# Kernel tuning notes

Hardware: AMD Instinct MI355X
Metric: run time of the kernel (lower is better)

Reference implementation:

```python
import jax, jax.numpy as jnp
import numpy as np

B, N, DIM = 64, 64, 256
HEADS, P = 4, 16
H, W, C = 56, 56, 256
CH = C // HEADS            # per-head channels = eff_in_dim = eff_out_dim = 64
IN_PTS = HEADS * P         # 64
OUT_PTS = IN_PTS           # 64
TOTAL = CH * CH + IN_PTS * OUT_PTS  # 8192
GRAD_NORM = 1.0 / H

# RestrictGradNorm: identity fwd, clamp grad in bwd
@jax.custom_vjp
def restrict_grad(x):
    return x

def _rg_fwd(x):
    return x, None

def _rg_bwd(_, g):
    return (jnp.clip(g, -GRAD_NORM, GRAD_NORM),)

restrict_grad.defvjp(_rg_fwd, _rg_bwd)


def grid_sample_bilinear(feat, grid):
    # feat [G,c,h,w], grid [G,Hg,Wg,2] in [-1,1]; align_corners=False, zeros padding
    G, c, h, w = feat.shape
    Hg, Wg = grid.shape[1], grid.shape[2]
    Q = Hg * Wg
    x = (grid[..., 0] + 1.0) * 0.5 * w - 0.5
    y = (grid[..., 1] + 1.0) * 0.5 * h - 0.5
    x0f = jnp.floor(x); y0f = jnp.floor(y)
    wx1 = x - x0f; wx0 = 1.0 - wx1
    wy1 = y - y0f; wy0 = 1.0 - wy1
    x0 = x0f.astype(jnp.int32); y0 = y0f.astype(jnp.int32)
    fflat = feat.reshape(G, c, h * w)

    def gather(xi, yi):
        valid = (xi >= 0) & (xi < w) & (yi >= 0) & (yi < h)
        idx = (jnp.clip(yi, 0, h - 1) * w + jnp.clip(xi, 0, w - 1)).reshape(G, Q)
        v = jnp.take_along_axis(fflat, jnp.broadcast_to(idx[:, None, :], (G, c, Q)), axis=2)
        return v * valid.reshape(G, 1, Q)

    out = (gather(x0, y0) * (wx0 * wy0).reshape(G, 1, Q)
           + gather(x0 + 1, y0) * (wx1 * wy0).reshape(G, 1, Q)
           + gather(x0, y0 + 1) * (wx0 * wy1).reshape(G, 1, Q)
           + gather(x0 + 1, y0 + 1) * (wx1 * wy1).reshape(G, 1, Q))
    return out.reshape(G, c, Hg, Wg)


def setup_inputs() -> dict:
    key = jax.random.key(0)
    ks = jax.random.split(key, 10)
    img_feat = jax.random.normal(ks[0], (B, C, H, W), jnp.float32)
    ctr = jax.random.uniform(ks[1], (B, N, 2), jnp.float32) * 0.8 + 0.1
    wh = jax.random.uniform(ks[2], (B, N, 2), jnp.float32) * 0.4 + 0.1
    token_roi = jnp.concatenate([ctr - wh / 2, ctr + wh / 2], axis=-1)
    query = jax.random.normal(ks[3], (B, N, DIM), jnp.float32)
    W_off = jax.random.normal(ks[4], (DIM, HEADS * P * 2), jnp.float32) * 0.02
    b_off = jnp.zeros((HEADS * P * 2,), jnp.float32)
    ln_w = jnp.ones((DIM,), jnp.float32)
    ln_b = jnp.zeros((DIM,), jnp.float32)
    W1 = jax.random.normal(ks[5], (DIM, DIM // 4), jnp.float32) * 0.02
    b1 = jnp.zeros((DIM // 4,), jnp.float32)
    W2 = jax.random.normal(ks[6], (DIM // 4, TOTAL), jnp.float32) * 0.02
    b2 = jax.random.normal(ks[7], (TOTAL,), jnp.float32) * 0.02
    m_beta = jnp.zeros((CH,), jnp.float32)
    s_beta = jnp.zeros((OUT_PTS,), jnp.float32)
    W_out = jax.random.normal(ks[8], (CH * OUT_PTS, DIM), jnp.float32) * 0.02
    b_out = jnp.zeros((DIM,), jnp.float32)
    return dict(img_feat=img_feat, token_roi=token_roi, query=query, W_off=W_off,
                b_off=b_off, ln_w=ln_w, ln_b=ln_b, W1=W1, b1=b1, W2=W2, b2=b2,
                m_beta=m_beta, s_beta=s_beta, W_out=W_out, b_out=b_out)


def _forward(img_feat, token_roi, query, W_off, b_off, ln_w, ln_b, W1, b1, W2, b2,
             m_beta, s_beta, W_out, b_out):
    # 1) sampling offsets from query
    off = (query @ W_off + b_off).reshape(B, N, 1, IN_PTS, 2)
    # 2) make_absolute_sampling_point: normalize over points (unbiased std, as torch)
    mean = off.mean(axis=-2, keepdims=True)
    std = jnp.std(off, axis=-2, ddof=1, keepdims=True) + 1e-7
    off = (off - mean) / (3.0 * std)
    roi_xy = (token_roi[:, :, 2:] + token_roi[:, :, :2]) * 0.5   # [B,N,2]
    roi_wh = token_roi[:, :, 2:] - token_roi[:, :, :2]
    pts = roi_xy[:, :, None, None, :] + off * roi_wh[:, :, None, None, :]  # [B,N,1,HP,2]
    # 3) sampling_from_img_feat: per-head bilinear grid sample
    sp = pts.reshape(B, N, 1, HEADS, P, 2).transpose(0, 3, 1, 2, 4, 5)
    sp = sp.reshape(B * HEADS, N, P, 2)
    sp = restrict_grad(sp)
    grid = sp * 2.0 - 1.0
    feat = img_feat.reshape(B * HEADS, CH, H, W)
    out = grid_sample_bilinear(feat, grid)                        # [B*HEADS, CH, N, P]
    out = out.reshape(B, HEADS, CH, N, 1, P).transpose(0, 3, 4, 1, 5, 2)
    sampled = out.reshape(B * N, IN_PTS, CH)                      # g==1 in AdaptiveMixing
    # 4) AdaptiveMixing: parameter generator (LN eps 1e-6 -> Linear -> Linear)
    mu = query.mean(-1, keepdims=True)
    var = query.var(-1, keepdims=True)
    qn = (query - mu) / jnp.sqrt(var + 1e-6) * ln_w + ln_b
    params = ((qn @ W1 + b1) @ W2 + b2).reshape(B * N, TOTAL)
    cm = params[:, :CH * CH].reshape(B * N, CH, CH)               # channel mixing
    sm = params[:, CH * CH:].reshape(B * N, OUT_PTS, IN_PTS)      # spatial mixing
    x = jax.nn.gelu(jnp.einsum('bpc,bcd->bpd', sampled, cm) + m_beta, approximate=False)
    x = jax.nn.gelu(jnp.einsum('bop,bpc->boc', sm, x) + s_beta[None, :, None], approximate=False)
    x = x.reshape(B, N, OUT_PTS * CH) @ W_out + b_out
    return x


def reference(img_feat, token_roi, query, W_off, b_off, ln_w, ln_b, W1, b1, W2, b2,
              m_beta, s_beta, W_out, b_out):
    return _forward(img_feat, token_roi, query, W_off, b_off, ln_w, ln_b, W1, b1,
                    W2, b2, m_beta, s_beta, W_out, b_out)
```

## Files before the change

### kernel.cpp

```cpp
#include <hip/hip_runtime.h>


typedef unsigned short u16;
typedef u16 u16x8 __attribute__((ext_vector_type(8)));
typedef u16 u16x4 __attribute__((ext_vector_type(4)));
typedef short bf16x8 __attribute__((ext_vector_type(8)));
typedef float f32x4 __attribute__((ext_vector_type(4)));
#define SA 72
#define MFMA(a, b, c) __builtin_amdgcn_mfma_f32_16x16x32_bf16(a, b, c, 0, 0, 0)

static __device__ __forceinline__ float bf2f(u16 s) {
    union { float f; unsigned u; } v; v.u = ((unsigned)s) << 16; return v.f;
}
static __device__ __forceinline__ u16 f2bf(float f) {
    union { float f; unsigned u; } v; v.f = f;
    unsigned r = v.u + 0x7fffu + ((v.u >> 16) & 1u);
    return (u16)(r >> 16);
}
static __device__ __forceinline__ float gelu(float x) {
    const float z  = x * 0.70710678118654752f;
    const float az = fabsf(z);
    const float t  = 1.0f / fmaf(0.3275911f, az, 1.0f);
    float p = fmaf(t, 1.061405429f, -1.453152027f);
    p = fmaf(t, p, 1.421413741f);
    p = fmaf(t, p, -0.284496736f);
    p = fmaf(t, p, 0.254829592f);
    p = p * t;
    const float e    = __expf(-z * z);
    const float erfa = fmaf(-p, e, 1.0f);
    const float erfz = copysignf(erfa, z);
    return 0.5f * x * (1.0f + erfz);
}
static __device__ __forceinline__ float loadf(const void* p, size_t i, int isbf) {
    return isbf ? bf2f(((const u16*)p)[i]) : ((const float*)p)[i];
}
static __device__ __forceinline__ int detect_bf(const void* ln_w) {
    return (*(const unsigned*)ln_w == 0x3F800000u) ? 0 : 1;
}


static __device__ void body_trans(const void* __restrict__ src, u16* __restrict__ dst,
                                  int R, int C, int c0, int r0, int isbf,
                                  float* __restrict__ tile) {
    const int tid = threadIdx.x;
#pragma unroll
    for (int i = 0; i < 16; i++) {
        int e = i * 256 + tid;
        int rr = e >> 6, cc = e & 63;
        tile[rr * 65 + cc] = loadf(src, (size_t)(r0 + rr) * C + c0 + cc, isbf);
    }
    __syncthreads();
#pragma unroll
    for (int i = 0; i < 16; i++) {
        int e = i * 256 + tid;
        int cc = e >> 6, rr = e & 63;
        dst[(size_t)(c0 + cc) * R + r0 + rr] = f2bf(tile[rr * 65 + cc]);
    }
}

static __device__ void body_k0(const void* __restrict__ img, u16* __restrict__ featT,
                               int pos0, int c0, int bz, int isbf,
                               u16* __restrict__ tile ) {
    const int tid = threadIdx.x;
    if (isbf) {
        const u16* ib = (const u16*)img;
#pragma unroll
        for (int i = 0; i < 2; i++) {
            const int e = i * 256 + tid;
            const int ch = e >> 3, g = e & 7;
            const int gs = g ^ (ch & 7) ^ ((ch >> 3) & 7);
            u16x8 v = *(const u16x8*)&ib[((size_t)bz * 256 + c0 + ch) * 3136 + pos0 + g * 8];
            *(u16x8*)&tile[ch * SA + gs * 8] = v;
        }
    } else {
        const float* ifp = (const float*)img;
#pragma unroll
        for (int i = 0; i < 4; i++) {
            const int e = i * 256 + tid;
            const int ch = e >> 4, pq = (e & 15) * 4;
            const int g = pq >> 3, gs = g ^ (ch & 7) ^ ((ch >> 3) & 7);
            f32x4 v = *(const f32x4*)&ifp[((size_t)bz * 256 + c0 + ch) * 3136 + pos0 + pq];
            u16x4 o;
#pragma unroll
            for (int j = 0; j < 4; j++) o[j] = f2bf(v[j]);
            *(u16x4*)&tile[ch * SA + gs * 8 + (pq & 7)] = o;
        }
    }
    __syncthreads();
#pragma unroll
    for (int i = 0; i < 2; i++) {
        const int e = i * 256 + tid;
        const int pos = e >> 3, cb = (e & 7) * 8;
        const int pg = pos >> 3, pe = pos & 7;
        u16x8 v;
#pragma unroll
        for (int j = 0; j < 8; j++) {
            const int row = cb + j;
            const int sw = pg ^ (row & 7) ^ ((row >> 3) & 7);
            v[j] = tile[row * SA + sw * 8 + pe];
        }
        *(u16x8*)&featT[((size_t)bz * 3136 + pos0 + pos) * 256 + c0 + cb] = v;
    }
}

static __device__ void body_k1(const void* __restrict__ query, const void* __restrict__ roi,
                               const void* __restrict__ W_off, const void* __restrict__ b_off,
                               const void* __restrict__ ln_w, const void* __restrict__ ln_b,
                               const void* __restrict__ W1, const void* __restrict__ b1,
                               int isbf, int t,
                               float* __restrict__ pts, u16* __restrict__ hbuf,
                               float* __restrict__ smem) {
    float* qf    = smem;
    float* qn    = smem + 256;
    float* offl  = smem + 512;
    float* red   = smem + 640;
    float* stats = smem + 648;
    const int tid = threadIdx.x;
    float q = loadf(query, (size_t)t * 256 + tid, isbf);
    qf[tid] = q;
    float v = q;
#pragma unroll
    for (int o = 32; o; o >>= 1) v += __shfl_down(v, o, 64);
    if ((tid & 63) == 0) red[tid >> 6] = v;
    __syncthreads();
    if (tid == 0) stats[0] = (red[0] + red[1] + red[2] + red[3]) * (1.f / 256.f);
    __syncthreads();
    float mu = stats[0];
    float dv = q - mu;
    v = dv * dv;
#pragma unroll
    for (int o = 32; o; o >>= 1) v += __shfl_down(v, o, 64);
    if ((tid & 63) == 0) red[tid >> 6] = v;
    __syncthreads();
    if (tid == 0) stats[1] = (red[0] + red[1] + red[2] + red[3]) * (1.f / 256.f);
    __syncthreads();
    float inv = rsqrtf(stats[1] + 1e-6f);
    qn[tid] = dv * inv * loadf(ln_w, tid, isbf) + loadf(ln_b, tid, isbf);
    __syncthreads();
    if (tid < 128) {
        float a0 = 0.f, a1 = 0.f, a2 = 0.f, a3 = 0.f;
        for (int d = 0; d < 256; d += 4) {
            a0 = fmaf(qf[d],     loadf(W_off, (size_t)d * 128 + tid, isbf),       a0);
            a1 = fmaf(qf[d + 1], loadf(W_off, (size_t)(d + 1) * 128 + tid, isbf), a1);
            a2 = fmaf(qf[d + 2], loadf(W_off, (size_t)(d + 2) * 128 + tid, isbf), a2);
            a3 = fmaf(qf[d + 3], loadf(W_off, (size_t)(d + 3) * 128 + tid, isbf), a3);
        }
        offl[tid] = ((a0 + a1) + (a2 + a3)) + loadf(b_off, tid, isbf);
    } else if (tid < 192) {
        int k = tid - 128;
        float a0 = 0.f, a1 = 0.f, a2 = 0.f, a3 = 0.f;
        for (int d = 0; d < 256; d += 4) {
            a0 = fmaf(qn[d],     loadf(W1, (size_t)d * 64 + k, isbf),       a0);
            a1 = fmaf(qn[d + 1], loadf(W1, (size_t)(d + 1) * 64 + k, isbf), a1);
            a2 = fmaf(qn[d + 2], loadf(W1, (size_t)(d + 2) * 64 + k, isbf), a2);
            a3 = fmaf(qn[d + 3], loadf(W1, (size_t)(d + 3) * 64 + k, isbf), a3);
        }
        hbuf[(size_t)t * 64 + k] = f2bf(((a0 + a1) + (a2 + a3)) + loadf(b1, k, isbf));
    }
    __syncthreads();
    const float ov = (tid < 128) ? offl[tid] : 0.f;
    {
        float s = ov;
#pragma unroll
        for (int o = 2; o < 64; o <<= 1) s += __shfl_xor(s, o, 64);
        if (tid < 128 && (tid & 63) < 2) red[(tid >> 6) * 2 + (tid & 1)] = s;
    }
    __syncthreads();
    const int xy = tid & 1;
    const float m = (red[xy] + red[2 + xy]) * (1.f / 64.f);
    {
        float d = (tid < 128) ? ov - m : 0.f;
        float sq = d * d;
#pragma unroll
        for (int o = 2; o < 64; o <<= 1) sq += __shfl_xor(sq, o, 64);
        if (tid < 128 && (tid & 63) < 2) red[4 + (tid >> 6) * 2 + (tid & 1)] = sq;
    }
    __syncthreads();
    if (tid < 128) {
        float s2 = red[4 + xy] + red[6 + xy];
        float sd = sqrtf(s2 * (1.f / 63.f));
        float inv3 = 1.f / (3.f * (sd + 1e-7f));
        float lo = loadf(roi, (size_t)t * 4 + xy, isbf);
        float hi = loadf(roi, (size_t)t * 4 + 2 + xy, isbf);
        pts[(size_t)t * 128 + tid] = 0.5f * (lo + hi) + (ov - m) * inv3 * (hi - lo);
    }
}

static __device__ void body_k2t(const u16* __restrict__ featT, const float* __restrict__ pts,
                                u16* __restrict__ sampled, int t) {
    const int tid = threadIdx.x;
    const int pt = tid >> 2, cg = tid & 3;
    const int b = t >> 6, hh = pt >> 4;
    const float px = pts[(size_t)t * 128 + pt * 2], py = pts[(size_t)t * 128 + pt * 2 + 1];
    const float x = px * 56.f - 0.5f, y = py * 56.f - 0.5f;
    const float x0f = floorf(x), y0f = floorf(y);
    const int ix0 = (int)x0f, iy0 = (int)y0f;
    const float wx1 = x - x0f, wx0 = 1.f - wx1, wy1 = y - y0f, wy0 = 1.f - wy1;
    float acc[16];
#pragma unroll
    for (int i = 0; i < 16; i++) acc[i] = 0.f;
    const int chbase = hh * 64 + cg * 16;
#pragma unroll
    for (int corner = 0; corner < 4; corner++) {
        const int xi = ix0 + (corner & 1), yi = iy0 + (corner >> 1);
        const bool ok = (xi >= 0) & (xi < 56) & (yi >= 0) & (yi < 56);
        const float wgt = ok ? ((corner & 1) ? wx1 : wx0) * ((corner >> 1) ? wy1 : wy0) : 0.f;
        const int xc = min(max(xi, 0), 55), yc = min(max(yi, 0), 55);
        const u16x8* p8 = (const u16x8*)&featT[((size_t)b * 3136 + yc * 56 + xc) * 256 + chbase];
        u16x8 a = p8[0], c = p8[1];
#pragma unroll
        for (int i = 0; i < 8; i++) {
            acc[i]     = fmaf(wgt, bf2f(a[i]), acc[i]);
            acc[8 + i] = fmaf(wgt, bf2f(c[i]), acc[8 + i]);
        }
    }
    u16x8 o0, o1;
#pragma unroll
    for (int i = 0; i < 8; i++) { o0[i] = f2bf(acc[i]); o1[i] = f2bf(acc[8 + i]); }
    u16x8* q8 = (u16x8*)&sampled[(size_t)t * 4096 + pt * 64 + cg * 16];
    q8[0] = o0; q8[1] = o1;
}

static __device__ void body_k2d(const void* __restrict__ img, const float* __restrict__ pts,
                                u16* __restrict__ sampled, int t, int isbf) {
    const int tid = threadIdx.x;
    const int pt = tid >> 2, cg = tid & 3;
    const int b = t >> 6, hh = pt >> 4;
    const float px = pts[(size_t)t * 128 + pt * 2], py = pts[(size_t)t * 128 + pt * 2 + 1];
    const float x = px * 56.f - 0.5f, y = py * 56.f - 0.5f;
    const float x0f = floorf(x), y0f = floorf(y);
    const int ix0 = (int)x0f, iy0 = (int)y0f;
    const float wx1 = x - x0f, wx0 = 1.f - wx1, wy1 = y - y0f, wy0 = 1.f - wy1;
    float acc[16];
#pragma unroll
    for (int i = 0; i < 16; i++) acc[i] = 0.f;
    const int chbase = b * 256 + hh * 64 + cg * 16;
#pragma unroll
    for (int corner = 0; corner < 4; corner++) {
        const int xi = ix0 + (corner & 1), yi = iy0 + (corner >> 1);
        const bool ok = (xi >= 0) & (xi < 56) & (yi >= 0) & (yi < 56);
        const float wgt = ok ? ((corner & 1) ? wx1 : wx0) * ((corner >> 1) ? wy1 : wy0) : 0.f;
        const int xc = min(max(xi, 0), 55), yc = min(max(yi, 0), 55);
        const size_t sp = yc * 56 + xc;
#pragma unroll
        for (int i = 0; i < 16; i++)
            acc[i] = fmaf(wgt, loadf(img, ((size_t)(chbase + i)) * 3136 + sp, isbf), acc[i]);
    }
    for (int i = 0; i < 16; i++)
        sampled[(size_t)t * 4096 + pt * 64 + cg * 16 + i] = f2bf(acc[i]);
}

static __device__ void body_k4(const u16* __restrict__ hb, const u16* __restrict__ W2T,
                               const void* __restrict__ b2, int isbf,
                               u16* __restrict__ params, int m0, int n0,
                               u16* __restrict__ As, u16* __restrict__ Bs) {
    const int tid = threadIdx.x;
    const int lane = tid & 63, w = tid >> 6;
    const int wm = w & 1, wn = w >> 1;
    const int l16 = lane & 15, quad = lane >> 4;
    {
        const int row = tid >> 2, kp = (tid & 3) * 16;
        const u16x8* ga = (const u16x8*)&hb[(size_t)(m0 + row) * 64 + kp];
        *(u16x8*)&As[row * SA + kp]     = ga[0];
        *(u16x8*)&As[row * SA + kp + 8] = ga[1];
        const u16x8* gb = (const u16x8*)&W2T[(size_t)(n0 + row) * 64 + kp];
        *(u16x8*)&Bs[row * SA + kp]     = gb[0];
        *(u16x8*)&Bs[row * SA + kp + 8] = gb[1];
    }
    __syncthreads();
    f32x4 acc[2][2];
#pragma unroll
    for (int i = 0; i < 2; i++)
#pragma unroll
        for (int j = 0; j < 2; j++) acc[i][j] = (f32x4){0.f, 0.f, 0.f, 0.f};
#pragma unroll
    for (int kk = 0; kk < 64; kk += 32) {
        bf16x8 af[2], bfr[2];
        af[0]  = *(const bf16x8*)&As[(wm * 32 + l16) * SA + kk + quad * 8];
        af[1]  = *(const bf16x8*)&As[(wm * 32 + 16 + l16) * SA + kk + quad * 8];
        bfr[0] = *(const bf16x8*)&Bs[(wn * 32 + l16) * SA + kk + quad * 8];
        bfr[1] = *(const bf16x8*)&Bs[(wn * 32 + 16 + l16) * SA + kk + quad * 8];
#pragma unroll
        for (int tm = 0; tm < 2; tm++)
#pragma unroll
            for (int tn = 0; tn < 2; tn++)
                acc[tm][tn] = MFMA(af[tm], bfr[tn], acc[tm][tn]);
    }
    float bb[2];
    bb[0] = loadf(b2, n0 + wn * 32 + l16, isbf);
    bb[1] = loadf(b2, n0 + wn * 32 + 16 + l16, isbf);
#pragma unroll
    for (int tm = 0; tm < 2; tm++)
#pragma unroll
        for (int tn = 0; tn < 2; tn++)
#pragma unroll
            for (int r = 0; r < 4; r++) {
                int row = m0 + wm * 32 + tm * 16 + quad * 4 + r;
                int col = n0 + wn * 32 + tn * 16 + l16;
                params[(size_t)row * 8192 + col] = f2bf(acc[tm][tn][r] + bb[tn]);
            }
}

__global__ __launch_bounds__(256) void kA(const void* __restrict__ img,
        const void* __restrict__ roi, const void* __restrict__ query,
        const void* __restrict__ W_off, const void* __restrict__ b_off,
        const void* __restrict__ ln_w, const void* __restrict__ ln_b,
        const void* __restrict__ W1, const void* __restrict__ b1,
        const void* __restrict__ W2, const void* __restrict__ W_out,
        u16* __restrict__ featT, float* __restrict__ pts, u16* __restrict__ hbuf,
        u16* __restrict__ W2T, u16* __restrict__ WoutT, int nk0) {
    __shared__ __align__(16) float smem[64 * 65];
    const int bi = blockIdx.x;
    const int isbf = detect_bf(ln_w);
    if (bi < 4096) {
        body_k1(query, roi, W_off, b_off, ln_w, ln_b, W1, b1, isbf, bi, pts, hbuf, smem);
    } else if (bi < 4096 + nk0) {
        const int i = bi - 4096;
        const int pos0 = (i % 49) * 64, c0 = ((i / 49) & 3) * 64, bz = i / 196;
        body_k0(img, featT, pos0, c0, bz, isbf, (u16*)smem);
    } else if (bi < 4096 + nk0 + 128) {
        const int j = bi - 4096 - nk0;
        body_trans(W2, W2T, 64, 8192, j * 64, 0, isbf, smem);
    } else {
        const int j = bi - 4096 - nk0 - 128;
        body_trans(W_out, WoutT, 4096, 256, (j & 3) * 64, (j >> 2) * 64, isbf, smem);
    }
}

__global__ __launch_bounds__(256) void kB(const u16* __restrict__ featT,
        const void* __restrict__ img, const float* __restrict__ pts,
        const u16* __restrict__ hbuf, const u16* __restrict__ W2T,
        const void* __restrict__ b2, const void* __restrict__ ln_w,
        u16* __restrict__ sampled, u16* __restrict__ params, int tierA) {
    __shared__ u16 AB[2][64 * SA];
    const int bi = blockIdx.x;
    if (bi < 4096) {
        if (tierA) body_k2t(featT, pts, sampled, bi);
        else       body_k2d(img, pts, sampled, bi, detect_bf(ln_w));
    } else {
        const int isbf = detect_bf(ln_w);
        const int i = bi - 4096;
        const int m0 = (i & 63) * 64, n0 = (i >> 6) * 64;
        body_k4(hbuf, W2T, b2, isbf, params, m0, n0, AB[0], AB[1]);
    }
}

__global__ __launch_bounds__(256) void k5_mfma(const u16* __restrict__ params,
        const void* __restrict__ m_beta, const void* __restrict__ s_beta,
        const void* __restrict__ ln_w, u16* __restrict__ sampled) {
    __shared__ u16 S[64 * SA];
    __shared__ u16 CMT[64 * SA];
    __shared__ u16 SM[64 * SA];
    __shared__ u16 X1T[64 * SA];
    const int t = blockIdx.x, tid = threadIdx.x;
    const int isbf = detect_bf(ln_w);
    const size_t pbase = (size_t)t * 8192, sbase = (size_t)t * 4096;
    const int lane = tid & 63, w = tid >> 6;
    const int wm = w & 1, wn = w >> 1;
    const int l16 = lane & 15, quad = lane >> 4;
    {
        const int r = tid >> 2, cp = (tid & 3) * 16;
        const u16x8* gs = (const u16x8*)&sampled[sbase + r * 64 + cp];
        *(u16x8*)&S[r * SA + cp]     = gs[0];
        *(u16x8*)&S[r * SA + cp + 8] = gs[1];
        const u16x8* gm = (const u16x8*)&params[pbase + 4096 + r * 64 + cp];
        *(u16x8*)&SM[r * SA + cp]     = gm[0];
        *(u16x8*)&SM[r * SA + cp + 8] = gm[1];
    }
    {
        const int d = tid & 63, cp = (tid >> 6) * 16;
        u16x8 b0, b1;
#pragma unroll
        for (int j = 0; j < 8; j++) {
            b0[j] = params[pbase + (size_t)(cp + j) * 64 + d];
            b1[j] = params[pbase + (size_t)(cp + 8 + j) * 64 + d];
        }
        *(u16x8*)&CMT[d * SA + cp]     = b0;
        *(u16x8*)&CMT[d * SA + cp + 8] = b1;
    }
    __syncthreads();
    f32x4 acc[2][2];
#pragma unroll
    for (int i = 0; i < 2; i++)
#pragma unroll
        for (int j = 0; j < 2; j++) acc[i][j] = (f32x4){0.f, 0.f, 0.f, 0.f};
#pragma unroll
    for (int kk = 0; kk < 64; kk += 32) {
        bf16x8 af[2], bfr[2];
        af[0]  = *(const bf16x8*)&S[(wm * 32 + l16) * SA + kk + quad * 8];
        af[1]  = *(const bf16x8*)&S[(wm * 32 + 16 + l16) * SA + kk + quad * 8];
        bfr[0] = *(const bf16x8*)&CMT[(wn * 32 + l16) * SA + kk + quad * 8];
        bfr[1] = *(const bf16x8*)&CMT[(wn * 32 + 16 + l16) * SA + kk + quad * 8];
#pragma unroll
        for (int tm = 0; tm < 2; tm++)
#pragma unroll
            for (int tn = 0; tn < 2; tn++)
                acc[tm][tn] = MFMA(af[tm], bfr[tn], acc[tm][tn]);
    }
    float mb[2];
    mb[0] = loadf(m_beta, wn * 32 + l16, isbf);
    mb[1] = loadf(m_beta, wn * 32 + 16 + l16, isbf);
#pragma unroll
    for (int tm = 0; tm < 2; tm++)
#pragma unroll
        for (int tn = 0; tn < 2; tn++)
#pragma unroll
            for (int r = 0; r < 4; r++) {
                int p = wm * 32 + tm * 16 + quad * 4 + r;
                int d = wn * 32 + tn * 16 + l16;
                X1T[d * SA + p] = f2bf(gelu(acc[tm][tn][r] + mb[tn]));
            }
    __syncthreads();
#pragma unroll
    for (int i = 0; i < 2; i++)
#pragma unroll
        for (int j = 0; j < 2; j++) acc[i][j] = (f32x4){0.f, 0.f, 0.f, 0.f};
#pragma unroll
    for (int kk = 0; kk < 64; kk += 32) {
        bf16x8 af[2], bfr[2];
        af[0]  = *(const bf16x8*)&SM[(wm * 32 + l16) * SA + kk + quad * 8];
        af[1]  = *(const bf16x8*)&SM[(wm * 32 + 16 + l16) * SA + kk + quad * 8];
        bfr[0] = *(const bf16x8*)&X1T[(wn * 32 + l16) * SA + kk + quad * 8];
        bfr[1] = *(const bf16x8*)&X1T[(wn * 32 + 16 + l16) * SA + kk + quad * 8];
#pragma unroll
        for (int tm = 0; tm < 2; tm++)
#pragma unroll
            for (int tn = 0; tn < 2; tn++)
                acc[tm][tn] = MFMA(af[tm], bfr[tn], acc[tm][tn]);
    }
#pragma unroll
    for (int tm = 0; tm < 2; tm++)
#pragma unroll
        for (int tn = 0; tn < 2; tn++)
#pragma unroll
            for (int r = 0; r < 4; r++) {
                int o = wm * 32 + tm * 16 + quad * 4 + r;
                int d = wn * 32 + tn * 16 + l16;
                float sb = loadf(s_beta, o, isbf);
                sampled[sbase + o * 64 + d] = f2bf(gelu(acc[tm][tn][r] + sb));
            }
}

__global__ __launch_bounds__(256) void k6_mfma(const u16* __restrict__ x2b,
        const u16* __restrict__ WoutT, float* __restrict__ part) {
    __shared__ u16 As[2][64 * SA];
    __shared__ u16 Bs[2][64 * SA];
    const int tid = threadIdx.x;
    const int m0 = blockIdx.x * 64, n0 = blockIdx.y * 64, kz = blockIdx.z;
    const int lane = tid & 63, w = tid >> 6;
    const int wm = w & 1, wn = w >> 1;
    const int l16 = lane & 15, quad = lane >> 4;
    const int sRow = tid >> 2, sK = (tid & 3) * 16;
    const u16* aRow = &x2b[(size_t)(m0 + sRow) * 4096 + kz * 1024 + sK];
    const u16* bRow = &WoutT[(size_t)(n0 + sRow) * 4096 + kz * 1024 + sK];
    f32x4 acc[2][2];
#pragma unroll
    for (int i = 0; i < 2; i++)
#pragma unroll
        for (int j = 0; j < 2; j++) acc[i][j] = (f32x4){0.f, 0.f, 0.f, 0.f};
    u16x8 ra0 = ((const u16x8*)aRow)[0], ra1 = ((const u16x8*)aRow)[1];
    u16x8 rb0 = ((const u16x8*)bRow)[0], rb1 = ((const u16x8*)bRow)[1];
#pragma unroll
    for (int it = 0; it < 16; ++it) {
        const int cur = it & 1;
        *(u16x8*)&As[cur][sRow * SA + sK]     = ra0;
        *(u16x8*)&As[cur][sRow * SA + sK + 8] = ra1;
        *(u16x8*)&Bs[cur][sRow * SA + sK]     = rb0;
        *(u16x8*)&Bs[cur][sRow * SA + sK + 8] = rb1;
        __syncthreads();
        if (it + 1 < 16) {
            const u16* an = aRow + (it + 1) * 64;
            const u16* bn = bRow + (it + 1) * 64;
            ra0 = ((const u16x8*)an)[0]; ra1 = ((const u16x8*)an)[1];
            rb0 = ((const u16x8*)bn)[0]; rb1 = ((const u16x8*)bn)[1];
        }
#pragma unroll
        for (int kk = 0; kk < 64; kk += 32) {
            bf16x8 af[2], bfr[2];
            af[0]  = *(const bf16x8*)&As[cur][(wm * 32 + l16) * SA + kk + quad * 8];
            af[1]  = *(const bf16x8*)&As[cur][(wm * 32 + 16 + l16) * SA + kk + quad * 8];
            bfr[0] = *(const bf16x8*)&Bs[cur][(wn * 32 + l16) * SA + kk + quad * 8];
            bfr[1] = *(const bf16x8*)&Bs[cur][(wn * 32 + 16 + l16) * SA + kk + quad * 8];
#pragma unroll
            for (int tm = 0; tm < 2; tm++)
#pragma unroll
                for (int tn = 0; tn < 2; tn++)
                    acc[tm][tn] = MFMA(af[tm], bfr[tn], acc[tm][tn]);
        }
    }
    float* pbase = part + (size_t)kz * (4096 * 256);
#pragma unroll
    for (int tm = 0; tm < 2; tm++)
#pragma unroll
        for (int tn = 0; tn < 2; tn++)
#pragma unroll
            for (int r = 0; r < 4; r++) {
                int row = m0 + wm * 32 + tm * 16 + quad * 4 + r;
                int col = n0 + wn * 32 + tn * 16 + l16;
                pbase[(size_t)row * 256 + col] = acc[tm][tn][r];
            }
}

__global__ void k7_reduce(const float* __restrict__ part, const void* __restrict__ b_out,
                          const void* __restrict__ ln_w, float* __restrict__ out) {
    const int i = blockIdx.x * 256 + threadIdx.x;
    const int isbf = detect_bf(ln_w);
    out[i] = part[i] + part[1048576 + i] + part[2 * 1048576 + i] + part[3 * 1048576 + i]
           + loadf(b_out, i & 255, isbf);
}

extern "C" void kernel_launch(void* const* d_in, const int* in_sizes, int n_in,
                              void* d_out, int out_size, void* d_ws, size_t ws_size,
                              hipStream_t stream) {
    const void* img    = d_in[0];
    const void* roi    = d_in[1];
    const void* query  = d_in[2];
    const void* W_off  = d_in[3];
    const void* b_off  = d_in[4];
    const void* ln_w   = d_in[5];
    const void* ln_b   = d_in[6];
    const void* W1     = d_in[7];
    const void* b1     = d_in[8];
    const void* W2     = d_in[9];
    const void* b2     = d_in[10];
    const void* m_beta = d_in[11];
    const void* s_beta = d_in[12];
    const void* W_out  = d_in[13];
    const void* b_out  = d_in[14];

    char* ws = (char*)d_ws;
    float* pts     = (float*)(ws + 1024);
    u16*   hbuf    = (u16*)(ws + 2098176);
    u16*   sampled = (u16*)(ws + 2622464);
    u16*   params  = (u16*)(ws + 36176896);
    u16*   W2T     = (u16*)(ws + 103285760);
    u16*   WoutT   = (u16*)(ws + 104334336);
    float* part    = (float*)(ws + 106431488);
    u16*   featT   = (u16*)(ws + 123208704);
    const bool tierA = ws_size >= (size_t)225969152;
    const int nk0 = tierA ? 12544 : 0;

    kA<<<4096 + nk0 + 384, 256, 0, stream>>>(img, roi, query, W_off, b_off, ln_w, ln_b,
                                             W1, b1, W2, W_out, featT, pts, hbuf,
                                             W2T, WoutT, nk0);
    kB<<<12288, 256, 0, stream>>>(featT, img, pts, hbuf, W2T, b2, ln_w,
                                  sampled, params, tierA ? 1 : 0);
    k5_mfma<<<4096, 256, 0, stream>>>(params, m_beta, s_beta, ln_w, sampled);
    k6_mfma<<<dim3(64, 4, 4), 256, 0, stream>>>(sampled, WoutT, part);
    k7_reduce<<<4096, 256, 0, stream>>>(part, b_out, ln_w, (float*)d_out);
}
```

Before: 489.8 us.

## Stage MFMA outputs through LDS for vectorized stores and split kA launch

The params GEMM epilogue now writes results plus bias into an LDS tile, then emits coalesced 16-byte bf16 stores instead of scattered 2-byte stores. k5 loads the channel-mixing block with vector loads into LDS and transposes it there instead of doing strided global gathers. It caches s_beta in shared memory and stages the final output through LDS for vectorized stores. The fused kA launch is split into a small-LDS query/offset kernel and a separate feature/weight transpose kernel, so the first part can run at higher occupancy. The cost is extra barriers and one additional kernel launch.

```diff
diff --git a/kernel.cpp b/kernel.cpp
--- a/kernel.cpp
+++ b/kernel.cpp
@@ -253,11 +253,14 @@
 static __device__ void body_k4(const u16* __restrict__ hb, const u16* __restrict__ W2T,
                                const void* __restrict__ b2, int isbf,
                                u16* __restrict__ params, int m0, int n0,
-                               u16* __restrict__ As, u16* __restrict__ Bs) {
+                               u16* __restrict__ AB, float* __restrict__ bbias) {
+    u16* As = AB;
+    u16* Bs = AB + 64 * SA;
     const int tid = threadIdx.x;
     const int lane = tid & 63, w = tid >> 6;
     const int wm = w & 1, wn = w >> 1;
     const int l16 = lane & 15, quad = lane >> 4;
+    if (tid < 64) bbias[tid] = loadf(b2, n0 + tid, isbf);
     {
         const int row = tid >> 2, kp = (tid & 3) * 16;
         const u16x8* ga = (const u16x8*)&hb[(size_t)(m0 + row) * 64 + kp];
@@ -286,43 +289,57 @@
             for (int tn = 0; tn < 2; tn++)
                 acc[tm][tn] = MFMA(af[tm], bfr[tn], acc[tm][tn]);
     }
-    float bb[2];
-    bb[0] = loadf(b2, n0 + wn * 32 + l16, isbf);
-    bb[1] = loadf(b2, n0 + wn * 32 + 16 + l16, isbf);
+    __syncthreads();
+    float* Cf = (float*)AB;
 #pragma unroll
     for (int tm = 0; tm < 2; tm++)
 #pragma unroll
         for (int tn = 0; tn < 2; tn++)
 #pragma unroll
             for (int r = 0; r < 4; r++) {
-                int row = m0 + wm * 32 + tm * 16 + quad * 4 + r;
-                int col = n0 + wn * 32 + tn * 16 + l16;
-                params[(size_t)row * 8192 + col] = f2bf(acc[tm][tn][r] + bb[tn]);
+                int row = wm * 32 + tm * 16 + quad * 4 + r;
+                int col = wn * 32 + tn * 16 + l16;
+                Cf[row * 68 + col] = acc[tm][tn][r] + bbias[col];
             }
-}
-
-__global__ __launch_bounds__(256) void kA(const void* __restrict__ img,
-        const void* __restrict__ roi, const void* __restrict__ query,
-        const void* __restrict__ W_off, const void* __restrict__ b_off,
-        const void* __restrict__ ln_w, const void* __restrict__ ln_b,
-        const void* __restrict__ W1, const void* __restrict__ b1,
+    __syncthreads();
+    {
+        const int row = tid >> 2, cq = (tid & 3) * 16;
+        u16x8 o0, o1;
+#pragma unroll
+        for (int j = 0; j < 8; j++) {
+            o0[j] = f2bf(Cf[row * 68 + cq + j]);
+            o1[j] = f2bf(Cf[row * 68 + cq + 8 + j]);
+        }
+        u16x8* q8 = (u16x8*)&params[(size_t)(m0 + row) * 8192 + n0 + cq];
+        q8[0] = o0; q8[1] = o1;
+    }
+}
+
+__global__ __launch_bounds__(256) void kA1(const void* __restrict__ query,
+        const void* __restrict__ roi, const void* __restrict__ W_off,
+        const void* __restrict__ b_off, const void* __restrict__ ln_w,
+        const void* __restrict__ ln_b, const void* __restrict__ W1,
+        const void* __restrict__ b1, float* __restrict__ pts, u16* __restrict__ hbuf) {
+    __shared__ float smem[656];
+    body_k1(query, roi, W_off, b_off, ln_w, ln_b, W1, b1, detect_bf(ln_w),
+            blockIdx.x, pts, hbuf, smem);
+}
+
+__global__ __launch_bounds__(256) void kA0(const void* __restrict__ img,
         const void* __restrict__ W2, const void* __restrict__ W_out,
-        u16* __restrict__ featT, float* __restrict__ pts, u16* __restrict__ hbuf,
+        const void* __restrict__ ln_w, u16* __restrict__ featT,
         u16* __restrict__ W2T, u16* __restrict__ WoutT, int nk0) {
     __shared__ __align__(16) float smem[64 * 65];
     const int bi = blockIdx.x;
     const int isbf = detect_bf(ln_w);
-    if (bi < 4096) {
-        body_k1(query, roi, W_off, b_off, ln_w, ln_b, W1, b1, isbf, bi, pts, hbuf, smem);
-    } else if (bi < 4096 + nk0) {
-        const int i = bi - 4096;
-        const int pos0 = (i % 49) * 64, c0 = ((i / 49) & 3) * 64, bz = i / 196;
+    if (bi < nk0) {
+        const int pos0 = (bi % 49) * 64, c0 = ((bi / 49) & 3) * 64, bz = bi / 196;
         body_k0(img, featT, pos0, c0, bz, isbf, (u16*)smem);
-    } else if (bi < 4096 + nk0 + 128) {
-        const int j = bi - 4096 - nk0;
+    } else if (bi < nk0 + 128) {
+        const int j = bi - nk0;
         body_trans(W2, W2T, 64, 8192, j * 64, 0, isbf, smem);
     } else {
-        const int j = bi - 4096 - nk0 - 128;
+        const int j = bi - nk0 - 128;
         body_trans(W_out, WoutT, 4096, 256, (j & 3) * 64, (j >> 2) * 64, isbf, smem);
     }
 }
@@ -332,7 +349,8 @@
         const u16* __restrict__ hbuf, const u16* __restrict__ W2T,
         const void* __restrict__ b2, const void* __restrict__ ln_w,
         u16* __restrict__ sampled, u16* __restrict__ params, int tierA) {
-    __shared__ u16 AB[2][64 * SA];
+    __shared__ u16 AB[2 * 64 * SA];
+    __shared__ float bbias[64];
     const int bi = blockIdx.x;
     if (bi < 4096) {
         if (tierA) body_k2t(featT, pts, sampled, bi);
@@ -341,7 +359,7 @@
         const int isbf = detect_bf(ln_w);
         const int i = bi - 4096;
         const int m0 = (i & 63) * 64, n0 = (i >> 6) * 64;
-        body_k4(hbuf, W2T, b2, isbf, params, m0, n0, AB[0], AB[1]);
+        body_k4(hbuf, W2T, b2, isbf, params, m0, n0, AB, bbias);
     }
 }
 
@@ -352,12 +370,14 @@
     __shared__ u16 CMT[64 * SA];
     __shared__ u16 SM[64 * SA];
     __shared__ u16 X1T[64 * SA];
+    __shared__ float sbl[64];
     const int t = blockIdx.x, tid = threadIdx.x;
     const int isbf = detect_bf(ln_w);
     const size_t pbase = (size_t)t * 8192, sbase = (size_t)t * 4096;
     const int lane = tid & 63, w = tid >> 6;
     const int wm = w & 1, wn = w >> 1;
     const int l16 = lane & 15, quad = lane >> 4;
+    if (tid < 64) sbl[tid] = loadf(s_beta, tid, isbf);
     {
         const int r = tid >> 2, cp = (tid & 3) * 16;
         const u16x8* gs = (const u16x8*)&sampled[sbase + r * 64 + cp];
@@ -366,14 +386,18 @@
         const u16x8* gm = (const u16x8*)&params[pbase + 4096 + r * 64 + cp];
         *(u16x8*)&SM[r * SA + cp]     = gm[0];
         *(u16x8*)&SM[r * SA + cp + 8] = gm[1];
-    }
+        const u16x8* gc = (const u16x8*)&params[pbase + r * 64 + cp];
+        *(u16x8*)&X1T[r * SA + cp]     = gc[0];
+        *(u16x8*)&X1T[r * SA + cp + 8] = gc[1];
+    }
+    __syncthreads();
     {
         const int d = tid & 63, cp = (tid >> 6) * 16;
         u16x8 b0, b1;
 #pragma unroll
         for (int j = 0; j < 8; j++) {
-            b0[j] = params[pbase + (size_t)(cp + j) * 64 + d];
-            b1[j] = params[pbase + (size_t)(cp + 8 + j) * 64 + d];
+            b0[j] = X1T[(cp + j) * SA + d];
+            b1[j] = X1T[(cp + 8 + j) * SA + d];
         }
         *(u16x8*)&CMT[d * SA + cp]     = b0;
         *(u16x8*)&CMT[d * SA + cp + 8] = b1;
@@ -400,6 +424,7 @@
     float mb[2];
     mb[0] = loadf(m_beta, wn * 32 + l16, isbf);
     mb[1] = loadf(m_beta, wn * 32 + 16 + l16, isbf);
+    __syncthreads();
 #pragma unroll
     for (int tm = 0; tm < 2; tm++)
 #pragma unroll
@@ -428,6 +453,7 @@
             for (int tn = 0; tn < 2; tn++)
                 acc[tm][tn] = MFMA(af[tm], bfr[tn], acc[tm][tn]);
     }
+    __syncthreads();
 #pragma unroll
     for (int tm = 0; tm < 2; tm++)
 #pragma unroll
@@ -436,9 +462,16 @@
             for (int r = 0; r < 4; r++) {
                 int o = wm * 32 + tm * 16 + quad * 4 + r;
                 int d = wn * 32 + tn * 16 + l16;
-                float sb = loadf(s_beta, o, isbf);
-                sampled[sbase + o * 64 + d] = f2bf(gelu(acc[tm][tn][r] + sb));
+                S[o * SA + d] = f2bf(gelu(acc[tm][tn][r] + sbl[o]));
             }
+    __syncthreads();
+    {
+        const int r = tid >> 2, cp = (tid & 3) * 16;
+        u16x8 v0 = *(u16x8*)&S[r * SA + cp];
+        u16x8 v1 = *(u16x8*)&S[r * SA + cp + 8];
+        u16x8* q8 = (u16x8*)&sampled[sbase + r * 64 + cp];
+        q8[0] = v0; q8[1] = v1;
+    }
 }
 
 __global__ __launch_bounds__(256) void k6_mfma(const u16* __restrict__ x2b,
@@ -540,9 +573,9 @@
     const bool tierA = ws_size >= (size_t)225969152;
     const int nk0 = tierA ? 12544 : 0;
 
-    kA<<<4096 + nk0 + 384, 256, 0, stream>>>(img, roi, query, W_off, b_off, ln_w, ln_b,
-                                             W1, b1, W2, W_out, featT, pts, hbuf,
-                                             W2T, WoutT, nk0);
+    kA1<<<4096, 256, 0, stream>>>(query, roi, W_off, b_off, ln_w, ln_b, W1, b1,
+                                  pts, hbuf);
+    kA0<<<nk0 + 384, 256, 0, stream>>>(img, W2, W_out, ln_w, featT, W2T, WoutT, nk0);
     kB<<<12288, 256, 0, stream>>>(featT, img, pts, hbuf, W2T, b2, ln_w,
                                   sampled, params, tierA ? 1 : 0);
     k5_mfma<<<4096, 256, 0, stream>>>(params, m_beta, s_beta, ln_w, sampled);
```

After: 498.3 us. No clear change (+1.7%).
